# Performance work log

Measured on AMD Instinct MI355X. Metric: run time of the kernel, lower is better.

Reference implementation:

```python
import jax, jax.numpy as jnp
import numpy as np

EPS_GN = 1e-8
EPS_ATTN = 1e-8


def setup_inputs() -> dict:
    key = jax.random.key(0)
    ks = jax.random.split(key, 13)
    B, C, N = 4, 512, 2048
    s = 0.02
    return {
        "x": jax.random.normal(ks[0], (B, C, N), jnp.float32),
        "dw_w": jax.random.normal(ks[1], (C, 3), jnp.float32) * s,
        "pw_w": jax.random.normal(ks[2], (C, C), jnp.float32) * s,
        "u_w": jax.random.normal(ks[3], (2 * C, C), jnp.float32) * s,
        "u_b": jax.random.normal(ks[4], (2 * C,), jnp.float32) * s,
        "v_w": jax.random.normal(ks[5], (2 * C, C), jnp.float32) * s,
        "v_b": jax.random.normal(ks[6], (2 * C,), jnp.float32) * s,
        "h_w": jax.random.normal(ks[7], (C, C), jnp.float32) * s,
        "h_b": jax.random.normal(ks[8], (C,), jnp.float32) * s,
        "q_w": jax.random.normal(ks[9], (C, C), jnp.float32) * s,
        "k_w": jax.random.normal(ks[10], (C, C), jnp.float32) * s,
        "o_w": jax.random.normal(ks[11], (C, 2 * C), jnp.float32) * s,
        "o_b": jax.random.normal(ks[12], (C,), jnp.float32) * s,
    }


def reference(x, dw_w, pw_w, u_w, u_b, v_w, v_b, h_w, h_b, q_w, k_w, o_w, o_b):
    # x: [B, C, N]
    C = x.shape[1]
    # GroupNorm(1, C): normalize over (C, N) per sample; affine is identity-init
    # in torch but we follow the module math with default weight=1, bias=0
    mean = jnp.mean(x, axis=(1, 2), keepdims=True)
    var = jnp.var(x, axis=(1, 2), keepdims=True)
    z = (x - mean) * jax.lax.rsqrt(var + EPS_GN)

    # local depthwise conv k=3, pad=1 (cross-correlation), no bias
    zp = jnp.pad(z, ((0, 0), (0, 0), (1, 1)))
    dw = (dw_w[:, 0, None] * zp[:, :, :-2]
          + dw_w[:, 1, None] * zp[:, :, 1:-1]
          + dw_w[:, 2, None] * zp[:, :, 2:])
    # pointwise conv (no bias)
    z = z + jnp.einsum('oc,bcn->bon', pw_w, dw)

    u = jax.nn.sigmoid(jnp.einsum('oc,bcn->bon', u_w, z) + u_b[:, None])  # [B,2C,N]
    v = jnp.einsum('oc,bcn->bon', v_w, z) + v_b[:, None]                  # [B,2C,N]
    h = jnp.einsum('oc,bcn->bno', h_w, z) + h_b                           # [B,N,C]

    q = h @ q_w.T  # [B,N,C]
    k = h @ k_w.T  # [B,N,C]
    scale = 1.0 / jnp.sqrt(jnp.float32(C))

    logits = jnp.einsum('bnc,bmc->bnm', q, k) * scale
    a = jax.nn.relu(logits)
    a = a * a
    a = a / (jnp.sum(a, axis=-1, keepdims=True) + EPS_ATTN)

    av = jnp.einsum('bnm,bom->bon', a, v)  # [B,2C,N]
    y = jnp.einsum('oc,bcn->bon', o_w, u * av) + o_b[:, None]
    return x + y
```

## Files before the change

### kernel.cpp

```cpp
#include <hip/hip_runtime.h>
#include <hip/hip_bf16.h>
#include <cstdint>

typedef __bf16 bhalf;
typedef __bf16 bhalf8 __attribute__((ext_vector_type(8)));
typedef float f32x4 __attribute__((ext_vector_type(4)));

enum { EPI_Z2=0, EPI_UV=1, EPI_BIAS=2, EPI_QK=3, EPI_ATTN=4, EPI_PV=5, EPI_Y=6 };

__device__ __forceinline__ void gl_lds16(const bhalf* g, bhalf* l) {
  __builtin_amdgcn_global_load_lds(
      (const __attribute__((address_space(1))) unsigned int*)g,
      (__attribute__((address_space(3))) unsigned int*)l,
      16, 0, 0);
}
__device__ __forceinline__ void barrier_raw() { asm volatile("s_barrier" ::: "memory"); }
#define VMW(n)  asm volatile("s_waitcnt vmcnt(" #n ")" ::: "memory")
#define LGKM0() asm volatile("s_waitcnt lgkmcnt(0)" ::: "memory")


template<int EPI>
__global__ void __launch_bounds__(512, 2)
gA(const bhalf* __restrict__ A, const bhalf* __restrict__ Bw,
   void* __restrict__ Out, void* __restrict__ Out2,
   const float* __restrict__ bias, const float* __restrict__ bias2,
   int N, int K, long sA, long sB, long sO, long sAuxf, float scale)
{
  constexpr int KSL = 256*64;
  constexpr int REG = 2*KSL;
  constexpr int DBUF = 2*REG;
  __shared__ __align__(16) char lds[2*DBUF];

  const int gx = gridDim.x, gy = gridDim.y;
  const int nwg = gx*gy;
  const int flat = blockIdx.y*gx + blockIdx.x;
  const int q8 = nwg>>3, r8 = nwg&7, xcd = flat&7, o8 = flat>>3;
  const int wsw = (xcd<r8 ? xcd*(q8+1) : r8*(q8+1)+(xcd-r8)*q8) + o8;
  const int bx = wsw % gx, by = wsw / gx;
  const int m0 = by*256, n0 = bx*256;
  const int bz = blockIdx.z;

  const bhalf* Ab = A + (long)bz*sA;
  const bhalf* Bb = Bw + (long)bz*sB;

  const int tid = threadIdx.x, wid = tid>>6, lane = tid&63;
  const int lm = lane&15, kq = lane>>4;
  const int wm = wid>>2, wn = wid&3;
  const int srow = lane>>2;
  const int csw = ((lane&3) ^ ((lane>>3)&3)) * 8;
  const int kqs = kq ^ ((lm>>1)&3);

  f32x4 acc[8][4];
  #pragma unroll
  for (int i=0;i<8;i++)
    #pragma unroll
    for (int j=0;j<4;j++) acc[i][j] = f32x4{0.f,0.f,0.f,0.f};

  auto stageA = [&](int kt){
    char* base = lds + (kt&1)*DBUF;
    const int k0 = kt*64;
    #pragma unroll
    for (int h=0; h<2; h++)
      #pragma unroll
      for (int ksl=0; ksl<2; ksl++){
        bhalf* d = (bhalf*)(base + ksl*KSL + (h*128 + wid*16)*64);
        gl_lds16(Ab + (long)(m0 + h*128 + wid*16 + srow)*K + k0 + ksl*32 + csw, d);
      }
  };
  auto stageB = [&](int kt){
    char* base = lds + (kt&1)*DBUF + REG;
    const int k0 = kt*64;
    #pragma unroll
    for (int h=0; h<2; h++)
      #pragma unroll
      for (int ksl=0; ksl<2; ksl++){
        bhalf* d = (bhalf*)(base + ksl*KSL + (h*128 + wid*16)*64);
        gl_lds16(Bb + (long)(n0 + h*128 + wid*16 + srow)*K + k0 + ksl*32 + csw, d);
      }
  };

  bhalf8 af[4][2], bf[4][2];
  auto readA = [&](int kt, int ih){
    char* base = lds + (kt&1)*DBUF;
    #pragma unroll
    for (int i2=0;i2<4;i2++)
      #pragma unroll
      for (int ksl=0;ksl<2;ksl++)
        af[i2][ksl] = *(const bhalf8*)(base + ksl*KSL + (wm*128 + ih*64 + i2*16 + lm)*64 + kqs*16);
  };
  auto readB = [&](int kt, int jh){
    char* base = lds + (kt&1)*DBUF + REG;
    #pragma unroll
    for (int j2=0;j2<2;j2++)
      #pragma unroll
      for (int ksl=0;ksl<2;ksl++)
        bf[jh*2+j2][ksl] = *(const bhalf8*)(base + ksl*KSL + (wn*64 + jh*32 + j2*16 + lm)*64 + kqs*16);
  };
  auto mfma16 = [&](int ih, int jh){
    __builtin_amdgcn_s_setprio(1);
    #pragma unroll
    for (int i2=0;i2<4;i2++)
      #pragma unroll
      for (int j2=0;j2<2;j2++)
        #pragma unroll
        for (int ksl=0;ksl<2;ksl++)
          acc[ih*4+i2][jh*2+j2] = __builtin_amdgcn_mfma_f32_16x16x32_bf16(
              af[i2][ksl], bf[jh*2+j2][ksl], acc[ih*4+i2][jh*2+j2], 0,0,0);
    __builtin_amdgcn_s_setprio(0);
  };

  const int NT = K>>6;
  stageA(0); stageB(0); stageA(1);
  for (int kt=0; kt<NT; ++kt){
    if (kt==NT-1) { VMW(0); } else { VMW(4); }
    barrier_raw();
    readA(kt,0); readB(kt,0);
    if (kt+1<NT) stageB(kt+1);
    mfma16(0,0);
    barrier_raw();
    readB(kt,1);
    mfma16(0,1);
    barrier_raw();
    readA(kt,1);
    mfma16(1,0);
    barrier_raw();
    if (kt+2<NT) stageA(kt+2);
    mfma16(1,1);
  }
  barrier_raw();

  if constexpr (EPI==EPI_ATTN){
    float rs[8][4];
    #pragma unroll
    for (int i=0;i<8;i++)
      #pragma unroll
      for (int r=0;r<4;r++) rs[i][r]=0.f;
    #pragma unroll
    for (int i=0;i<8;i++){
      #pragma unroll
      for (int j=0;j<4;j++){
        const int lcol = wn*64 + j*16 + lm;
        #pragma unroll
        for (int r=0;r<4;r++){
          const int lrow = wm*128 + i*16 + kq*4 + r;
          float v = acc[i][j][r];
          v *= scale; v = fmaxf(v,0.f); v = v*v;
          rs[i][r] += v;
          const int cb = lcol*2;
          const int lb = lrow*512 + (((cb>>5) ^ ((lrow>>2)&3))<<5) + (cb&31);
          *(bhalf*)(lds + lb) = (bhalf)v;
        }
      }
    }
    float* rd = (float*)Out2;
    #pragma unroll
    for (int i=0;i<8;i++){
      const int rbase = m0 + wm*128 + i*16 + kq*4;
      #pragma unroll
      for (int r=0;r<4;r++){
        float s = rs[i][r];
        s += __shfl_xor(s,1); s += __shfl_xor(s,2);
        s += __shfl_xor(s,4); s += __shfl_xor(s,8);
        if (lm==0) atomicAdd(rd + (long)bz*sAuxf + rbase + r, s);
      }
    }
    LGKM0();
    barrier_raw();
    char* obase = (char*)Out + 2*((long)bz*sO + (long)m0*N + n0);
    const int ldb = N*2;
    #pragma unroll
    for (int it=0; it<16; ++it){
      const int g = (it*512 + tid)*16;
      const int row = g >> 9, off = g & 511;
      const int lb = row*512 + (((off>>5) ^ ((row>>2)&3))<<5) + (off&31);
      uint4 val = *(const uint4*)(lds + lb);
      *(uint4*)(obase + (long)row*ldb + off) = val;
    }
  }
  if constexpr (EPI==EPI_UV){
    const bool uh = n0 < 1024;
    const float* bv = uh ? bias : bias2;
    const int bc0 = uh ? n0 : n0-1024;
    #pragma unroll
    for (int i=0;i<8;i++){
      #pragma unroll
      for (int j=0;j<4;j++){
        const int lcol = wn*64 + j*16 + lm;
        #pragma unroll
        for (int r=0;r<4;r++){
          const int lrow = wm*128 + i*16 + kq*4 + r;
          float v = acc[i][j][r] + bv[bc0 + lcol];
          if (uh){
            v = 1.f/(1.f + __expf(-v));
            const int cb = lcol*2;
            const int lb = lrow*512 + (((cb>>5) ^ ((lrow>>2)&3))<<5) + (cb&31);
            *(bhalf*)(lds + lb) = (bhalf)v;
          } else {
            const int lb = lcol*512 + 2*(lrow ^ ((lcol&15)<<2));
            *(bhalf*)(lds + lb) = (bhalf)v;
          }
        }
      }
    }
    LGKM0();
    barrier_raw();
    if (uh){
      char* obase = (char*)Out + 2*((long)m0*1024 + n0);
      #pragma unroll
      for (int it=0; it<16; ++it){
        const int g = (it*512 + tid)*16;
        const int row = g >> 9, off = g & 511;
        const int lb = row*512 + (((off>>5) ^ ((row>>2)&3))<<5) + (off&31);
        uint4 val = *(const uint4*)(lds + lb);
        *(uint4*)(obase + (long)row*2048 + off) = val;
      }
    } else {
      char* vb = (char*)Out2 + 2*((long)(m0>>11)*1024*2048 + (long)(n0-1024)*2048 + (m0 & 2047));
      #pragma unroll
      for (int it=0; it<16; ++it){
        const int g = (it*512 + tid)*16;
        const int row = g >> 9, off = g & 511;
        const int t0 = off >> 1;
        const int s = (row&15)<<2;
        unsigned long long lo = *(const unsigned long long*)(lds + row*512 + 2*(t0^s));
        unsigned long long hi = *(const unsigned long long*)(lds + row*512 + 2*((t0+4)^s));
        char* dst = vb + (long)row*4096 + off;
        ((unsigned long long*)dst)[0] = lo;
        ((unsigned long long*)dst)[1] = hi;
      }
    }
  }
  (void)scale; (void)bias; (void)bias2; (void)N;
}

template<int EPI>
__global__ void __launch_bounds__(512, 2)
gB(const bhalf* __restrict__ A, const bhalf* __restrict__ Bw,
   void* __restrict__ Out, void* __restrict__ Out2,
   const bhalf* __restrict__ auxb, const float* __restrict__ auxf,
   int N, int K, long sB, float scale, int rowshift)
{
  constexpr int KSLA = 256*64;
  constexpr int KSLB = 128*64;
  constexpr int REGA = 2*KSLA;
  constexpr int DBUF = REGA + 2*KSLB;
  __shared__ __align__(16) char lds[3*DBUF];

  const int gx = gridDim.x, gy = gridDim.y;
  const int nwg = gx*gy;
  const int flat = blockIdx.y*gx + blockIdx.x;
  const int q8 = nwg>>3, r8 = nwg&7, xcd = flat&7, o8 = flat>>3;
  const int wsw = (xcd<r8 ? xcd*(q8+1) : r8*(q8+1)+(xcd-r8)*q8) + o8;
  const int bx = wsw % gx, by = wsw / gx;
  const int m0 = by*256, n0 = bx*128;

  const bhalf* Ab = A;
  const bhalf* Bb = Bw + (rowshift ? (long)(m0>>rowshift)*sB : 0);

  const int tid = threadIdx.x, wid = tid>>6, lane = tid&63;
  const int lm = lane&15, kq = lane>>4;
  const int wm = wid>>1, wn = wid&1;
  const int srow = lane>>2;
  const int csw = ((lane&3) ^ ((lane>>3)&3)) * 8;
  const int kqs = kq ^ ((lm>>1)&3);

  f32x4 acc[4][4];
  #pragma unroll
  for (int i=0;i<4;i++)
    #pragma unroll
    for (int j=0;j<4;j++) acc[i][j] = f32x4{0.f,0.f,0.f,0.f};

  auto stageAB = [&](int kt){
    char* base = lds + (kt%3)*DBUF;
    const int k0 = kt*64;
    #pragma unroll
    for (int h=0; h<2; h++)
      #pragma unroll
      for (int ksl=0; ksl<2; ksl++){
        bhalf* d = (bhalf*)(base + ksl*KSLA + (h*128 + wid*16)*64);
        gl_lds16(Ab + (long)(m0 + h*128 + wid*16 + srow)*K + k0 + ksl*32 + csw, d);
      }
    #pragma unroll
    for (int ksl=0; ksl<2; ksl++){
      bhalf* d = (bhalf*)(base + REGA + ksl*KSLB + (wid*16)*64);
      gl_lds16(Bb + (long)(n0 + wid*16 + srow)*K + k0 + ksl*32 + csw, d);
    }
  };

  bhalf8 af[4][2], bf[4][2];
  auto readA = [&](int kt){
    char* base = lds + (kt%3)*DBUF;
    #pragma unroll
    for (int i2=0;i2<4;i2++)
      #pragma unroll
      for (int ksl=0;ksl<2;ksl++)
        af[i2][ksl] = *(const bhalf8*)(base + ksl*KSLA + (wm*64 + i2*16 + lm)*64 + kqs*16);
  };
  auto readB = [&](int kt, int jh){
    char* base = lds + (kt%3)*DBUF + REGA;
    #pragma unroll
    for (int j2=0;j2<2;j2++)
      #pragma unroll
      for (int ksl=0;ksl<2;ksl++)
        bf[jh*2+j2][ksl] = *(const bhalf8*)(base + ksl*KSLB + (wn*64 + jh*32 + j2*16 + lm)*64 + kqs*16);
  };
  auto mfma16 = [&](int jh){
    __builtin_amdgcn_s_setprio(1);
    #pragma unroll
    for (int i2=0;i2<4;i2++)
      #pragma unroll
      for (int j2=0;j2<2;j2++)
        #pragma unroll
        for (int ksl=0;ksl<2;ksl++)
          acc[i2][jh*2+j2] = __builtin_amdgcn_mfma_f32_16x16x32_bf16(
              af[i2][ksl], bf[jh*2+j2][ksl], acc[i2][jh*2+j2], 0,0,0);
    __builtin_amdgcn_s_setprio(0);
  };

  const int NT = K>>6;
  stageAB(0); stageAB(1);
  for (int kt=0; kt<NT; ++kt){
    if (kt==NT-1) { VMW(0); } else { VMW(6); }
    barrier_raw();
    readA(kt); readB(kt,0);
    if (kt+2<NT) stageAB(kt+2);
    mfma16(0);
    barrier_raw();
    readB(kt,1);
    mfma16(1);
  }
  barrier_raw();

  char* obase; int ldb;
  if constexpr (EPI==EPI_PV){
    obase = (char*)Out + 2*((long)m0*1024 + n0); ldb = 2048;
  }
  if constexpr (EPI==EPI_QK){
    bool qh = n0 < 512;
    obase = (char*)(qh?Out:Out2) + 2*((long)m0*512 + (n0 - (qh?0:512)));
    ldb = 1024;
  }
  #pragma unroll
  for (int i=0;i<4;i++){
    #pragma unroll
    for (int j=0;j<4;j++){
      const int lcol = wn*64 + j*16 + lm;
      #pragma unroll
      for (int r=0;r<4;r++){
        const int lrow = wm*64 + i*16 + kq*4 + r;
        float v = acc[i][j][r];
        if constexpr (EPI==EPI_PV){
          const int rowg = m0 + lrow;
          float den = auxf[rowg];
          v *= __builtin_amdgcn_rcpf(den + 1e-8f);
          v *= (float)auxb[(long)rowg*1024 + n0 + lcol];
        }
        const int cb = lcol*2;
        const int lb = lrow*256 + (((cb>>5) ^ ((lrow>>2)&3))<<5) + (cb&31);
        *(bhalf*)(lds + lb) = (bhalf)v;
      }
    }
  }
  LGKM0();
  barrier_raw();
  #pragma unroll
  for (int it=0; it<8; ++it){
    const int g = (it*512 + tid)*16;
    const int row = g >> 8, off = g & 255;
    const int lb = row*256 + (((off>>5) ^ ((row>>2)&3))<<5) + (off&31);
    uint4 val = *(const uint4*)(lds + lb);
    *(uint4*)(obase + (long)row*ldb + off) = val;
  }
  (void)scale; (void)auxb; (void)auxf; (void)N;
}

template<int EPI>
__global__ void __launch_bounds__(256, 2)
g4k(const bhalf* __restrict__ A, const bhalf* __restrict__ Bw,
    void* __restrict__ Out,
    const float* __restrict__ bias,
    const bhalf* __restrict__ auxb,
    const float* __restrict__ xadd,
    int M, int N, int K)
{
  constexpr int KSL = 256*64;
  constexpr int DBUF = 2*KSL;
  __shared__ __align__(16) char lds[2*DBUF];

  const int gx = gridDim.x, gy = gridDim.y;
  const int nwg = gx*gy;
  const int flat = blockIdx.y*gx + blockIdx.x;
  const int q8 = nwg>>3, r8 = nwg&7, xcd = flat&7, o8 = flat>>3;
  const int w = (xcd<r8 ? xcd*(q8+1) : r8*(q8+1)+(xcd-r8)*q8) + o8;
  const int bx = w % gx, by = w / gx;
  const int m0 = by*128, n0 = bx*128;

  const int tid = threadIdx.x;
  const int wid = tid>>6, lane = tid&63;
  const int lm = lane&15, kq = lane>>4;
  const int wm = wid>>1, wn = wid&1;
  const int srow = lane>>2;
  const int csw = ((lane&3) ^ ((lane>>3)&3))*8;
  const int kqs = kq ^ ((lm>>1)&3);

  f32x4 acc[4][4];
  #pragma unroll
  for (int i=0;i<4;i++)
    #pragma unroll
    for (int j=0;j<4;j++) acc[i][j] = f32x4{0.f,0.f,0.f,0.f};

  auto stage = [&](int kt){
    char* base = lds + (kt&1)*DBUF;
    const int k0 = kt*64;
    #pragma unroll
    for (int c=0;c<4;c++){
      const int r0 = c*64 + wid*16;
      #pragma unroll
      for (int ksl=0; ksl<2; ksl++){
        bhalf* d = (bhalf*)(base + ksl*KSL + r0*64);
        const bhalf* g = (r0 < 128)
          ? A  + (long)(m0 + r0 + srow)*K + k0 + ksl*32 + csw
          : Bw + (long)(n0 + r0 - 128 + srow)*K + k0 + ksl*32 + csw;
        gl_lds16(g, d);
      }
    }
  };

  bhalf8 af[4][2], bf[4][2];
  auto readA = [&](int kt){
    char* base = lds + (kt&1)*DBUF;
    #pragma unroll
    for (int i2=0;i2<4;i2++)
      #pragma unroll
      for (int ksl=0;ksl<2;ksl++)
        af[i2][ksl] = *(const bhalf8*)(base + ksl*KSL + (wm*64 + i2*16 + lm)*64 + kqs*16);
  };
  auto readB = [&](int kt, int jh){
    char* base = lds + (kt&1)*DBUF;
    #pragma unroll
    for (int j2=0;j2<2;j2++)
      #pragma unroll
      for (int ksl=0;ksl<2;ksl++)
        bf[jh*2+j2][ksl] = *(const bhalf8*)(base + ksl*KSL + (128 + wn*64 + jh*32 + j2*16 + lm)*64 + kqs*16);
  };
  auto mfma16 = [&](int jh){
    __builtin_amdgcn_s_setprio(1);
    #pragma unroll
    for (int i2=0;i2<4;i2++)
      #pragma unroll
      for (int j2=0;j2<2;j2++)
        #pragma unroll
        for (int ksl=0;ksl<2;ksl++)
          acc[i2][jh*2+j2] = __builtin_amdgcn_mfma_f32_16x16x32_bf16(
              af[i2][ksl], bf[jh*2+j2][ksl], acc[i2][jh*2+j2], 0,0,0);
    __builtin_amdgcn_s_setprio(0);
  };

  const int NT = K>>6;
  stage(0); stage(1);
  for (int kt=0; kt<NT; ++kt){
    if (kt==NT-1) { VMW(0); } else { VMW(8); }
    barrier_raw();
    readA(kt); readB(kt,0);
    mfma16(0);
    barrier_raw();
    readB(kt,1);
    if (kt+2<NT) stage(kt+2);
    mfma16(1);
  }
  barrier_raw();

  if constexpr (EPI==EPI_Y){
    #pragma unroll
    for (int i=0;i<4;i++){
      #pragma unroll
      for (int j=0;j<4;j++){
        const int lcol = wn*64 + j*16 + lm;
        #pragma unroll
        for (int r=0;r<4;r++){
          const int lrow = wm*64 + i*16 + kq*4 + r;
          float v = acc[i][j][r] + bias[n0 + lcol];
          const int lb = lcol*512 + 4*(lrow ^ ((lcol&15)<<2));
          *(float*)(lds + lb) = v;
        }
      }
    }
    LGKM0();
    barrier_raw();
    const int b = m0 >> 11, nb = m0 & 2047;
    float* ob = (float*)Out + ((long)b*512 + n0)*2048 + nb;
    const float* xb = xadd + ((long)b*512 + n0)*2048 + nb;
    #pragma unroll
    for (int it=0; it<16; ++it){
      const int g = (it*256 + tid)*16;
      const int row = g >> 9, off = g & 511;
      const int t0 = off >> 2;
      const int s = (row&15)<<2;
      f32x4 vv = *(const f32x4*)(lds + row*512 + 4*(t0^s));
      f32x4 xx = *(const f32x4*)(xb + (long)row*2048 + t0);
      *(f32x4*)(ob + (long)row*2048 + t0) = vv + xx;
    }
  } else {
    char* obase = (char*)Out + 2*((long)m0*N + n0);
    const int ldb = N*2;
    #pragma unroll
    for (int i=0;i<4;i++){
      #pragma unroll
      for (int j=0;j<4;j++){
        const int lcol = wn*64 + j*16 + lm;
        #pragma unroll
        for (int r=0;r<4;r++){
          const int lrow = wm*64 + i*16 + kq*4 + r;
          float v = acc[i][j][r];
          if constexpr (EPI==EPI_Z2)
            v += (float)auxb[(long)(m0+lrow)*N + n0 + lcol];
          if constexpr (EPI==EPI_BIAS)
            v += bias[n0 + lcol];
          const int cb = lcol*2;
          const int lb = lrow*256 + (((cb>>5) ^ ((lrow>>2)&3))<<5) + (cb&31);
          *(bhalf*)(lds + lb) = (bhalf)v;
        }
      }
    }
    LGKM0();
    barrier_raw();
    #pragma unroll
    for (int it=0; it<8; ++it){
      const int g = (it*256 + tid)*16;
      const int row = g >> 8, off = g & 255;
      const int lb = row*256 + (((off>>5) ^ ((row>>2)&3))<<5) + (off&31);
      uint4 val = *(const uint4*)(lds + lb);
      *(uint4*)(obase + (long)row*ldb + off) = val;
    }
  }
  (void)M; (void)xadd; (void)bias; (void)auxb;
}

struct CvtArgs { const float* src[7]; bhalf* dst[7]; int n[7]; };
__global__ void cvt_multi(CvtArgs a) {
  int seg = blockIdx.y;
  int i = (blockIdx.x*256 + threadIdx.x)*4;
  if (i >= a.n[seg]) return;
  float4 f = *(const float4*)(a.src[seg] + i);
  bhalf* d = a.dst[seg] + i;
  d[0]=(bhalf)f.x; d[1]=(bhalf)f.y; d[2]=(bhalf)f.z; d[3]=(bhalf)f.w;
}

__global__ void gn_part(const float* __restrict__ x, float* __restrict__ ps, float* __restrict__ pss) {
  int b = blockIdx.y;
  const float* xb = x + (long)b*(512*2048);
  float s=0.f, ss=0.f;
  #pragma unroll
  for (int it=0; it<8; it++){
    int idx = ((it*128 + blockIdx.x)*256 + threadIdx.x)*4;
    float4 f = *(const float4*)(xb + idx);
    s  += f.x+f.y+f.z+f.w;
    ss += f.x*f.x+f.y*f.y+f.z*f.z+f.w*f.w;
  }
  for (int off=32; off; off>>=1){ s += __shfl_xor(s,off); ss += __shfl_xor(ss,off); }
  __shared__ float ls[4], lss[4];
  int wid = threadIdx.x>>6, lane = threadIdx.x&63;
  if (lane==0){ ls[wid]=s; lss[wid]=ss; }
  __syncthreads();
  if (threadIdx.x==0){
    s = ls[0]+ls[1]+ls[2]+ls[3]; ss = lss[0]+lss[1]+lss[2]+lss[3];
    ps[b*128 + blockIdx.x] = s; pss[b*128 + blockIdx.x] = ss;
  }
}

__global__ void gn_final(const float* __restrict__ ps, const float* __restrict__ pss,
                         float* __restrict__ stats) {
  int b = blockIdx.x;
  float s = ps[b*128 + threadIdx.x], ss = pss[b*128 + threadIdx.x];
  for (int off=32; off; off>>=1){ s += __shfl_xor(s,off); ss += __shfl_xor(ss,off); }
  __shared__ float l0[2], l1[2];
  int wid = threadIdx.x>>6, lane = threadIdx.x&63;
  if (lane==0){ l0[wid]=s; l1[wid]=ss; }
  __syncthreads();
  if (threadIdx.x==0){
    s = l0[0]+l0[1]; ss = l1[0]+l1[1];
    float mean = s*(1.f/1048576.f);
    float var  = ss*(1.f/1048576.f) - mean*mean;
    stats[b*2] = mean; stats[b*2+1] = rsqrtf(var + 1e-8f);
  }
}

__global__ void norm_dw_T(const float* __restrict__ x, const float* __restrict__ stats,
                          const float* __restrict__ dw_w,
                          bhalf* __restrict__ zT, bhalf* __restrict__ dwT) {
  int b = blockIdx.z, n0 = blockIdx.x*32, c0 = blockIdx.y*32;
  float mean = stats[b*2], rstd = stats[b*2+1];
  __shared__ float zs[32][35];
  int tx = threadIdx.x, ty = threadIdx.y;
  #pragma unroll
  for (int r=0;r<4;r++){
    int c = c0 + ty + r*8;
    for (int cc=tx; cc<34; cc+=32){
      int n = n0 - 1 + cc;
      float v = 0.f;
      if (n>=0 && n<2048) v = (x[((long)b*512 + c)*2048 + n] - mean)*rstd;
      zs[ty + r*8][cc] = v;
    }
  }
  __syncthreads();
  float w0 = dw_w[(c0+tx)*3+0], w1 = dw_w[(c0+tx)*3+1], w2 = dw_w[(c0+tx)*3+2];
  #pragma unroll
  for (int r=0;r<4;r++){
    int ln = ty + r*8;
    float z = zs[tx][ln+1];
    float d = w0*zs[tx][ln] + w1*zs[tx][ln+1] + w2*zs[tx][ln+2];
    long o = ((long)b*2048 + n0 + ln)*512 + c0 + tx;
    zT[o] = (bhalf)z; dwT[o] = (bhalf)d;
  }
}

extern "C" void kernel_launch(void* const* d_in, const int* in_sizes, int n_in,
                              void* d_out, int out_size, void* d_ws, size_t ws_size,
                              hipStream_t stream) {
  (void)in_sizes; (void)n_in; (void)out_size; (void)ws_size;
  const float* x    = (const float*)d_in[0];
  const float* dw_w = (const float*)d_in[1];
  const float* pw_w = (const float*)d_in[2];
  const float* u_w  = (const float*)d_in[3];
  const float* u_b  = (const float*)d_in[4];
  const float* v_w  = (const float*)d_in[5];
  const float* v_b  = (const float*)d_in[6];
  const float* h_w  = (const float*)d_in[7];
  const float* h_b  = (const float*)d_in[8];
  const float* q_w  = (const float*)d_in[9];
  const float* k_w  = (const float*)d_in[10];
  const float* o_w  = (const float*)d_in[11];
  const float* o_b  = (const float*)d_in[12];
  float* out = (float*)d_out;

  char* ws = (char*)d_ws;
  size_t off = 0;
  auto alloc = [&](size_t bytes) -> void* {
    void* p = ws + off; off = (off + bytes + 255) & ~(size_t)255; return p;
  };

  float* ps    = (float*)alloc(4*128*4);
  float* pss   = (float*)alloc(4*128*4);
  float* stats = (float*)alloc(4*2*4);
  float* rden  = (float*)alloc(4*2048*4);
  bhalf* wb_pw = (bhalf*)alloc(512*512*2);
  bhalf* wb_uv = (bhalf*)alloc((size_t)2048*512*2);
  bhalf* wb_h  = (bhalf*)alloc(512*512*2);
  bhalf* wb_qk = (bhalf*)alloc((size_t)1024*512*2);
  bhalf* wb_o  = (bhalf*)alloc((size_t)512*1024*2);
  const size_t ACT = (size_t)4*2048*512;
  bhalf* zT   = (bhalf*)alloc(ACT*2);
  bhalf* dwT  = (bhalf*)alloc(ACT*2);
  bhalf* z2T  = (bhalf*)alloc(ACT*2);
  bhalf* ub   = (bhalf*)alloc(ACT*2*2);
  bhalf* v_fm = (bhalf*)alloc(ACT*2*2);
  bhalf* hb   = (bhalf*)alloc(ACT*2);
  bhalf* wsc  = (bhalf*)alloc((size_t)4*2048*2048*2);
  bhalf* uav  = (bhalf*)alloc(ACT*2*2);
  bhalf* qb = zT;  bhalf* kb = dwT;

  hipMemsetAsync(rden, 0, 4*2048*4, stream);

  CvtArgs ca;
  ca.src[0]=pw_w; ca.dst[0]=wb_pw;           ca.n[0]=512*512;
  ca.src[1]=u_w;  ca.dst[1]=wb_uv;           ca.n[1]=1024*512;
  ca.src[2]=v_w;  ca.dst[2]=wb_uv+1024*512;  ca.n[2]=1024*512;
  ca.src[3]=h_w;  ca.dst[3]=wb_h;            ca.n[3]=512*512;
  ca.src[4]=q_w;  ca.dst[4]=wb_qk;           ca.n[4]=512*512;
  ca.src[5]=k_w;  ca.dst[5]=wb_qk+512*512;   ca.n[5]=512*512;
  ca.src[6]=o_w;  ca.dst[6]=wb_o;            ca.n[6]=512*1024;
  cvt_multi<<<dim3(512,7), 256, 0, stream>>>(ca);

  gn_part<<<dim3(128,4), 256, 0, stream>>>(x, ps, pss);
  gn_final<<<dim3(4), 128, 0, stream>>>(ps, pss, stats);

  norm_dw_T<<<dim3(64,16,4), dim3(32,8), 0, stream>>>(x, stats, dw_w, zT, dwT);

  const float iscl = 0.044194173824159216f;
  g4k<EPI_Z2><<<dim3(4,64,1), 256, 0, stream>>>(dwT, wb_pw, z2T,
      nullptr, zT, nullptr, 8192, 512, 512);
  gA<EPI_UV><<<dim3(8,32,1), 512, 0, stream>>>(z2T, wb_uv, ub, v_fm,
      u_b, v_b, 2048, 512, 0, 0, 0, 0, 0.f);
  g4k<EPI_BIAS><<<dim3(4,64,1), 256, 0, stream>>>(z2T, wb_h, hb,
      h_b, nullptr, nullptr, 8192, 512, 512);
  gB<EPI_QK><<<dim3(8,32,1), 512, 0, stream>>>(hb, wb_qk, qb, kb,
      nullptr, nullptr, 1024, 512, 0, 0.f, 0);
  gA<EPI_ATTN><<<dim3(8,8,4), 512, 0, stream>>>(qb, kb, wsc, rden,
      nullptr, nullptr, 2048, 512,
      (long)2048*512, (long)2048*512, (long)2048*2048, 2048, iscl);
  gB<EPI_PV><<<dim3(8,32,1), 512, 0, stream>>>(wsc, v_fm, uav, nullptr,
      ub, rden, 1024, 2048, (long)1024*2048, 0.f, 11);
  g4k<EPI_Y><<<dim3(4,64,1), 256, 0, stream>>>(uav, wb_o, out,
      o_b, nullptr, x, 8192, 512, 1024);
}
```

Measured before the change: 183.7 us.

## Rework gB GEMM to 4 waves with 128-row warp tiles and K=32 stages

The 512-thread 256x128 GEMM kernel used for QK projection and PV becomes a 256-thread variant. Each wave now computes a 128x64 sub-tile (8x4 MFMA accumulators), and every k-step stages a 32-wide K slice for A and B together in one 384-row LDS buffer. This raises per-wave register reuse and cuts the thread count per block, at the cost of double the accumulator registers, more loop iterations with a barrier each, and fewer waves to hide latency.

```diff
diff --git a/kernel.cpp b/kernel.cpp
--- a/kernel.cpp
+++ b/kernel.cpp
@@ -234,16 +234,13 @@
 }
 
 template<int EPI>
-__global__ void __launch_bounds__(512, 2)
-gB(const bhalf* __restrict__ A, const bhalf* __restrict__ Bw,
+__global__ void __launch_bounds__(256, 2)
+gw(const bhalf* __restrict__ A, const bhalf* __restrict__ Bw,
    void* __restrict__ Out, void* __restrict__ Out2,
    const bhalf* __restrict__ auxb, const float* __restrict__ auxf,
    int N, int K, long sB, float scale, int rowshift)
 {
-  constexpr int KSLA = 256*64;
-  constexpr int KSLB = 128*64;
-  constexpr int REGA = 2*KSLA;
-  constexpr int DBUF = REGA + 2*KSLB;
+  constexpr int DBUF = 384*64;
   __shared__ __align__(16) char lds[3*DBUF];
 
   const int gx = gridDim.x, gy = gridDim.y;
@@ -264,66 +261,57 @@
   const int csw = ((lane&3) ^ ((lane>>3)&3)) * 8;
   const int kqs = kq ^ ((lm>>1)&3);
 
-  f32x4 acc[4][4];
-  #pragma unroll
-  for (int i=0;i<4;i++)
+  f32x4 acc[8][4];
+  #pragma unroll
+  for (int i=0;i<8;i++)
     #pragma unroll
     for (int j=0;j<4;j++) acc[i][j] = f32x4{0.f,0.f,0.f,0.f};
 
-  auto stageAB = [&](int kt){
+  auto stage = [&](int kt){
     char* base = lds + (kt%3)*DBUF;
-    const int k0 = kt*64;
-    #pragma unroll
-    for (int h=0; h<2; h++)
-      #pragma unroll
-      for (int ksl=0; ksl<2; ksl++){
-        bhalf* d = (bhalf*)(base + ksl*KSLA + (h*128 + wid*16)*64);
-        gl_lds16(Ab + (long)(m0 + h*128 + wid*16 + srow)*K + k0 + ksl*32 + csw, d);
-      }
-    #pragma unroll
-    for (int ksl=0; ksl<2; ksl++){
-      bhalf* d = (bhalf*)(base + REGA + ksl*KSLB + (wid*16)*64);
-      gl_lds16(Bb + (long)(n0 + wid*16 + srow)*K + k0 + ksl*32 + csw, d);
-    }
-  };
-
-  bhalf8 af[4][2], bf[4][2];
+    const int k0 = kt*32;
+    #pragma unroll
+    for (int c=0;c<6;c++){
+      const int r0 = wid*96 + c*16;
+      bhalf* d = (bhalf*)(base + r0*64);
+      const bhalf* g = (r0 < 256)
+        ? Ab + (long)(m0 + r0 + srow)*K + k0 + csw
+        : Bb + (long)(n0 + r0 - 256 + srow)*K + k0 + csw;
+      gl_lds16(g, d);
+    }
+  };
+
+  bhalf8 af[8], bf[4];
   auto readA = [&](int kt){
     char* base = lds + (kt%3)*DBUF;
     #pragma unroll
-    for (int i2=0;i2<4;i2++)
-      #pragma unroll
-      for (int ksl=0;ksl<2;ksl++)
-        af[i2][ksl] = *(const bhalf8*)(base + ksl*KSLA + (wm*64 + i2*16 + lm)*64 + kqs*16);
+    for (int i=0;i<8;i++)
+      af[i] = *(const bhalf8*)(base + (wm*128 + i*16 + lm)*64 + kqs*16);
   };
   auto readB = [&](int kt, int jh){
-    char* base = lds + (kt%3)*DBUF + REGA;
+    char* base = lds + (kt%3)*DBUF;
     #pragma unroll
     for (int j2=0;j2<2;j2++)
-      #pragma unroll
-      for (int ksl=0;ksl<2;ksl++)
-        bf[jh*2+j2][ksl] = *(const bhalf8*)(base + ksl*KSLB + (wn*64 + jh*32 + j2*16 + lm)*64 + kqs*16);
+      bf[jh*2+j2] = *(const bhalf8*)(base + (256 + wn*64 + jh*32 + j2*16 + lm)*64 + kqs*16);
   };
   auto mfma16 = [&](int jh){
     __builtin_amdgcn_s_setprio(1);
     #pragma unroll
-    for (int i2=0;i2<4;i2++)
+    for (int i=0;i<8;i++)
       #pragma unroll
       for (int j2=0;j2<2;j2++)
-        #pragma unroll
-        for (int ksl=0;ksl<2;ksl++)
-          acc[i2][jh*2+j2] = __builtin_amdgcn_mfma_f32_16x16x32_bf16(
-              af[i2][ksl], bf[jh*2+j2][ksl], acc[i2][jh*2+j2], 0,0,0);
+        acc[i][jh*2+j2] = __builtin_amdgcn_mfma_f32_16x16x32_bf16(
+            af[i], bf[jh*2+j2], acc[i][jh*2+j2], 0,0,0);
     __builtin_amdgcn_s_setprio(0);
   };
 
-  const int NT = K>>6;
-  stageAB(0); stageAB(1);
+  const int NT = K>>5;
+  stage(0); stage(1);
   for (int kt=0; kt<NT; ++kt){
     if (kt==NT-1) { VMW(0); } else { VMW(6); }
     barrier_raw();
     readA(kt); readB(kt,0);
-    if (kt+2<NT) stageAB(kt+2);
+    if (kt+2<NT) stage(kt+2);
     mfma16(0);
     barrier_raw();
     readB(kt,1);
@@ -341,13 +329,13 @@
     ldb = 1024;
   }
   #pragma unroll
-  for (int i=0;i<4;i++){
+  for (int i=0;i<8;i++){
     #pragma unroll
     for (int j=0;j<4;j++){
       const int lcol = wn*64 + j*16 + lm;
       #pragma unroll
       for (int r=0;r<4;r++){
-        const int lrow = wm*64 + i*16 + kq*4 + r;
+        const int lrow = wm*128 + i*16 + kq*4 + r;
         float v = acc[i][j][r];
         if constexpr (EPI==EPI_PV){
           const int rowg = m0 + lrow;
@@ -364,8 +352,8 @@
   LGKM0();
   barrier_raw();
   #pragma unroll
-  for (int it=0; it<8; ++it){
-    const int g = (it*512 + tid)*16;
+  for (int it=0; it<16; ++it){
+    const int g = (it*256 + tid)*16;
     const int row = g >> 8, off = g & 255;
     const int lb = row*256 + (((off>>5) ^ ((row>>2)&3))<<5) + (off&31);
     uint4 val = *(const uint4*)(lds + lb);
@@ -683,12 +671,12 @@
       u_b, v_b, 2048, 512, 0, 0, 0, 0, 0.f);
   g4k<EPI_BIAS><<<dim3(4,64,1), 256, 0, stream>>>(z2T, wb_h, hb,
       h_b, nullptr, nullptr, 8192, 512, 512);
-  gB<EPI_QK><<<dim3(8,32,1), 512, 0, stream>>>(hb, wb_qk, qb, kb,
+  gw<EPI_QK><<<dim3(8,32,1), 256, 0, stream>>>(hb, wb_qk, qb, kb,
       nullptr, nullptr, 1024, 512, 0, 0.f, 0);
   gA<EPI_ATTN><<<dim3(8,8,4), 512, 0, stream>>>(qb, kb, wsc, rden,
       nullptr, nullptr, 2048, 512,
       (long)2048*512, (long)2048*512, (long)2048*2048, 2048, iscl);
-  gB<EPI_PV><<<dim3(8,32,1), 512, 0, stream>>>(wsc, v_fm, uav, nullptr,
+  gw<EPI_PV><<<dim3(8,32,1), 256, 0, stream>>>(wsc, v_fm, uav, nullptr,
       ub, rden, 1024, 2048, (long)1024*2048, 0.f, 11);
   g4k<EPI_Y><<<dim3(4,64,1), 256, 0, stream>>>(uav, wb_o, out,
       o_b, nullptr, x, 8192, 512, 1024);
```

Result: slower. 191.2 us (+4.1%).

## Fuse h projection into UV GEMM and split gB k-slices to cut registers

Applied to the files above, without the earlier changes.

Concatenates h_w after u_w and v_w in one weight buffer so a single gA launch with 10 column tiles computes u, v and h, removing the separate g4k launch and a second read of z2T. The epilogue routes three column segments to their outputs: sigmoid for u, a transposed store for v, and bias only for h. Separately, the gB main loop now loads and multiplies one k-slice at a time with smaller fragment arrays, which lowers register pressure at the cost of two extra barriers per k-tile.

```diff
diff --git a/kernel.cpp b/kernel.cpp
--- a/kernel.cpp
+++ b/kernel.cpp
@@ -6,7 +6,7 @@
 typedef __bf16 bhalf8 __attribute__((ext_vector_type(8)));
 typedef float f32x4 __attribute__((ext_vector_type(4)));
 
-enum { EPI_Z2=0, EPI_UV=1, EPI_BIAS=2, EPI_QK=3, EPI_ATTN=4, EPI_PV=5, EPI_Y=6 };
+enum { EPI_Z2=0, EPI_UVH=1, EPI_BIAS=2, EPI_QK=3, EPI_ATTN=4, EPI_PV=5, EPI_Y=6 };
 
 __device__ __forceinline__ void gl_lds16(const bhalf* g, bhalf* l) {
   __builtin_amdgcn_global_load_lds(
@@ -22,8 +22,9 @@
 template<int EPI>
 __global__ void __launch_bounds__(512, 2)
 gA(const bhalf* __restrict__ A, const bhalf* __restrict__ Bw,
-   void* __restrict__ Out, void* __restrict__ Out2,
+   void* __restrict__ Out, void* __restrict__ Out2, void* __restrict__ Out3,
    const float* __restrict__ bias, const float* __restrict__ bias2,
+   const float* __restrict__ bias3,
    int N, int K, long sA, long sB, long sO, long sAuxf, float scale)
 {
   constexpr int KSL = 256*64;
@@ -177,10 +178,10 @@
       *(uint4*)(obase + (long)row*ldb + off) = val;
     }
   }
-  if constexpr (EPI==EPI_UV){
-    const bool uh = n0 < 1024;
-    const float* bv = uh ? bias : bias2;
-    const int bc0 = uh ? n0 : n0-1024;
+  if constexpr (EPI==EPI_UVH){
+    const int seg = n0 >> 10;
+    const float* bv = (seg==0) ? bias : (seg==1) ? bias2 : bias3;
+    const int bc0 = n0 - ((seg==0) ? 0 : (seg==1) ? 1024 : 2048);
     #pragma unroll
     for (int i=0;i<8;i++){
       #pragma unroll
@@ -190,31 +191,21 @@
         for (int r=0;r<4;r++){
           const int lrow = wm*128 + i*16 + kq*4 + r;
           float v = acc[i][j][r] + bv[bc0 + lcol];
-          if (uh){
-            v = 1.f/(1.f + __expf(-v));
+          if (seg==1){
+            const int lb = lcol*512 + 2*(lrow ^ ((lcol&15)<<2));
+            *(bhalf*)(lds + lb) = (bhalf)v;
+          } else {
+            if (seg==0) v = 1.f/(1.f + __expf(-v));
             const int cb = lcol*2;
             const int lb = lrow*512 + (((cb>>5) ^ ((lrow>>2)&3))<<5) + (cb&31);
             *(bhalf*)(lds + lb) = (bhalf)v;
-          } else {
-            const int lb = lcol*512 + 2*(lrow ^ ((lcol&15)<<2));
-            *(bhalf*)(lds + lb) = (bhalf)v;
           }
         }
       }
     }
     LGKM0();
     barrier_raw();
-    if (uh){
-      char* obase = (char*)Out + 2*((long)m0*1024 + n0);
-      #pragma unroll
-      for (int it=0; it<16; ++it){
-        const int g = (it*512 + tid)*16;
-        const int row = g >> 9, off = g & 511;
-        const int lb = row*512 + (((off>>5) ^ ((row>>2)&3))<<5) + (off&31);
-        uint4 val = *(const uint4*)(lds + lb);
-        *(uint4*)(obase + (long)row*2048 + off) = val;
-      }
-    } else {
+    if (seg==1){
       char* vb = (char*)Out2 + 2*((long)(m0>>11)*1024*2048 + (long)(n0-1024)*2048 + (m0 & 2047));
       #pragma unroll
       for (int it=0; it<16; ++it){
@@ -228,9 +219,21 @@
         ((unsigned long long*)dst)[0] = lo;
         ((unsigned long long*)dst)[1] = hi;
       }
-    }
-  }
-  (void)scale; (void)bias; (void)bias2; (void)N;
+    } else {
+      char* obase; int ldb;
+      if (seg==0){ obase = (char*)Out + 2*((long)m0*1024 + n0); ldb = 2048; }
+      else       { obase = (char*)Out3 + 2*((long)m0*512 + (n0-2048)); ldb = 1024; }
+      #pragma unroll
+      for (int it=0; it<16; ++it){
+        const int g = (it*512 + tid)*16;
+        const int row = g >> 9, off = g & 511;
+        const int lb = row*512 + (((off>>5) ^ ((row>>2)&3))<<5) + (off&31);
+        uint4 val = *(const uint4*)(lds + lb);
+        *(uint4*)(obase + (long)row*ldb + off) = val;
+      }
+    }
+  }
+  (void)scale; (void)bias; (void)bias2; (void)bias3; (void)Out3; (void)N;
 }
 
 template<int EPI>
@@ -287,33 +290,27 @@
     }
   };
 
-  bhalf8 af[4][2], bf[4][2];
-  auto readA = [&](int kt){
+  bhalf8 af[4], bf[2];
+  auto readA = [&](int kt, int ksl){
     char* base = lds + (kt%3)*DBUF;
     #pragma unroll
     for (int i2=0;i2<4;i2++)
-      #pragma unroll
-      for (int ksl=0;ksl<2;ksl++)
-        af[i2][ksl] = *(const bhalf8*)(base + ksl*KSLA + (wm*64 + i2*16 + lm)*64 + kqs*16);
-  };
-  auto readB = [&](int kt, int jh){
+      af[i2] = *(const bhalf8*)(base + ksl*KSLA + (wm*64 + i2*16 + lm)*64 + kqs*16);
+  };
+  auto readB = [&](int kt, int jh, int ksl){
     char* base = lds + (kt%3)*DBUF + REGA;
     #pragma unroll
     for (int j2=0;j2<2;j2++)
-      #pragma unroll
-      for (int ksl=0;ksl<2;ksl++)
-        bf[jh*2+j2][ksl] = *(const bhalf8*)(base + ksl*KSLB + (wn*64 + jh*32 + j2*16 + lm)*64 + kqs*16);
-  };
-  auto mfma16 = [&](int jh){
+      bf[j2] = *(const bhalf8*)(base + ksl*KSLB + (wn*64 + jh*32 + j2*16 + lm)*64 + kqs*16);
+  };
+  auto mfma8 = [&](int jh){
     __builtin_amdgcn_s_setprio(1);
     #pragma unroll
     for (int i2=0;i2<4;i2++)
       #pragma unroll
       for (int j2=0;j2<2;j2++)
-        #pragma unroll
-        for (int ksl=0;ksl<2;ksl++)
-          acc[i2][jh*2+j2] = __builtin_amdgcn_mfma_f32_16x16x32_bf16(
-              af[i2][ksl], bf[jh*2+j2][ksl], acc[i2][jh*2+j2], 0,0,0);
+        acc[i2][jh*2+j2] = __builtin_amdgcn_mfma_f32_16x16x32_bf16(
+            af[i2], bf[j2], acc[i2][jh*2+j2], 0,0,0);
     __builtin_amdgcn_s_setprio(0);
   };
 
@@ -322,12 +319,18 @@
   for (int kt=0; kt<NT; ++kt){
     if (kt==NT-1) { VMW(0); } else { VMW(6); }
     barrier_raw();
-    readA(kt); readB(kt,0);
+    readA(kt,0); readB(kt,0,0);
     if (kt+2<NT) stageAB(kt+2);
-    mfma16(0);
-    barrier_raw();
-    readB(kt,1);
-    mfma16(1);
+    mfma8(0);
+    barrier_raw();
+    readB(kt,1,0);
+    mfma8(1);
+    barrier_raw();
+    readA(kt,1); readB(kt,0,1);
+    mfma8(0);
+    barrier_raw();
+    readB(kt,1,1);
+    mfma8(1);
   }
   barrier_raw();
 
@@ -643,11 +646,10 @@
   float* pss   = (float*)alloc(4*128*4);
   float* stats = (float*)alloc(4*2*4);
   float* rden  = (float*)alloc(4*2048*4);
-  bhalf* wb_pw = (bhalf*)alloc(512*512*2);
-  bhalf* wb_uv = (bhalf*)alloc((size_t)2048*512*2);
-  bhalf* wb_h  = (bhalf*)alloc(512*512*2);
-  bhalf* wb_qk = (bhalf*)alloc((size_t)1024*512*2);
-  bhalf* wb_o  = (bhalf*)alloc((size_t)512*1024*2);
+  bhalf* wb_pw  = (bhalf*)alloc(512*512*2);
+  bhalf* wb_uvh = (bhalf*)alloc((size_t)2560*512*2);
+  bhalf* wb_qk  = (bhalf*)alloc((size_t)1024*512*2);
+  bhalf* wb_o   = (bhalf*)alloc((size_t)512*1024*2);
   const size_t ACT = (size_t)4*2048*512;
   bhalf* zT   = (bhalf*)alloc(ACT*2);
   bhalf* dwT  = (bhalf*)alloc(ACT*2);
@@ -662,13 +664,13 @@
   hipMemsetAsync(rden, 0, 4*2048*4, stream);
 
   CvtArgs ca;
-  ca.src[0]=pw_w; ca.dst[0]=wb_pw;           ca.n[0]=512*512;
-  ca.src[1]=u_w;  ca.dst[1]=wb_uv;           ca.n[1]=1024*512;
-  ca.src[2]=v_w;  ca.dst[2]=wb_uv+1024*512;  ca.n[2]=1024*512;
-  ca.src[3]=h_w;  ca.dst[3]=wb_h;            ca.n[3]=512*512;
-  ca.src[4]=q_w;  ca.dst[4]=wb_qk;           ca.n[4]=512*512;
-  ca.src[5]=k_w;  ca.dst[5]=wb_qk+512*512;   ca.n[5]=512*512;
-  ca.src[6]=o_w;  ca.dst[6]=wb_o;            ca.n[6]=512*1024;
+  ca.src[0]=pw_w; ca.dst[0]=wb_pw;            ca.n[0]=512*512;
+  ca.src[1]=u_w;  ca.dst[1]=wb_uvh;           ca.n[1]=1024*512;
+  ca.src[2]=v_w;  ca.dst[2]=wb_uvh+1024*512;  ca.n[2]=1024*512;
+  ca.src[3]=h_w;  ca.dst[3]=wb_uvh+2048*512;  ca.n[3]=512*512;
+  ca.src[4]=q_w;  ca.dst[4]=wb_qk;            ca.n[4]=512*512;
+  ca.src[5]=k_w;  ca.dst[5]=wb_qk+512*512;    ca.n[5]=512*512;
+  ca.src[6]=o_w;  ca.dst[6]=wb_o;             ca.n[6]=512*1024;
   cvt_multi<<<dim3(512,7), 256, 0, stream>>>(ca);
 
   gn_part<<<dim3(128,4), 256, 0, stream>>>(x, ps, pss);
@@ -679,14 +681,12 @@
   const float iscl = 0.044194173824159216f;
   g4k<EPI_Z2><<<dim3(4,64,1), 256, 0, stream>>>(dwT, wb_pw, z2T,
       nullptr, zT, nullptr, 8192, 512, 512);
-  gA<EPI_UV><<<dim3(8,32,1), 512, 0, stream>>>(z2T, wb_uv, ub, v_fm,
-      u_b, v_b, 2048, 512, 0, 0, 0, 0, 0.f);
-  g4k<EPI_BIAS><<<dim3(4,64,1), 256, 0, stream>>>(z2T, wb_h, hb,
-      h_b, nullptr, nullptr, 8192, 512, 512);
+  gA<EPI_UVH><<<dim3(10,32,1), 512, 0, stream>>>(z2T, wb_uvh, ub, v_fm, hb,
+      u_b, v_b, h_b, 2560, 512, 0, 0, 0, 0, 0.f);
   gB<EPI_QK><<<dim3(8,32,1), 512, 0, stream>>>(hb, wb_qk, qb, kb,
       nullptr, nullptr, 1024, 512, 0, 0.f, 0);
-  gA<EPI_ATTN><<<dim3(8,8,4), 512, 0, stream>>>(qb, kb, wsc, rden,
-      nullptr, nullptr, 2048, 512,
+  gA<EPI_ATTN><<<dim3(8,8,4), 512, 0, stream>>>(qb, kb, wsc, rden, nullptr,
+      nullptr, nullptr, nullptr, 2048, 512,
       (long)2048*512, (long)2048*512, (long)2048*2048, 2048, iscl);
   gB<EPI_PV><<<dim3(8,32,1), 512, 0, stream>>>(wsc, v_fm, uav, nullptr,
       ub, rden, 1024, 2048, (long)1024*2048, 0.f, 11);
```

Result: slower. 195.7 us (+6.5%).
